# Kernel optimization log

Measured on AMD Instinct MI355X. Metric: run time of the kernel, lower is better.

Reference implementation:

```python
import jax, jax.numpy as jnp
import numpy as np

HIDDEN = 2048
N_HEADS = 16
N_KV_HEADS = 4
HEAD_DIM = HIDDEN // N_HEADS  # 128
BATCH = 2
SEQ = 2048


def setup_inputs() -> dict:
    key = jax.random.key(0)
    ks = jax.random.split(key, 10)
    s = 0.02
    return {
        "hidden_states": jax.random.normal(ks[0], (BATCH, SEQ, HIDDEN), jnp.float32),
        "attention_mask": jnp.ones((BATCH, SEQ), jnp.int32),
        # weights stored [in, out] so y = x @ W + b (transpose of torch layout)
        "Wq": jax.random.normal(ks[1], (HIDDEN, N_HEADS * HEAD_DIM), jnp.float32) * s,
        "bq": jnp.zeros((N_HEADS * HEAD_DIM,), jnp.float32),
        "Wk": jax.random.normal(ks[2], (HIDDEN, N_KV_HEADS * HEAD_DIM), jnp.float32) * s,
        "bk": jnp.zeros((N_KV_HEADS * HEAD_DIM,), jnp.float32),
        "Wv": jax.random.normal(ks[3], (HIDDEN, N_KV_HEADS * HEAD_DIM), jnp.float32) * s,
        "bv": jnp.zeros((N_KV_HEADS * HEAD_DIM,), jnp.float32),
        "Wo": jax.random.normal(ks[4], (N_HEADS * HEAD_DIM, HIDDEN), jnp.float32) * s,
        "bo": jnp.zeros((HIDDEN,), jnp.float32),
    }


def reference(hidden_states, attention_mask, Wq, bq, Wk, bk, Wv, bv, Wo, bo):
    B, S, _ = hidden_states.shape
    q = hidden_states @ Wq + bq  # [B,S,H*D]
    k = hidden_states @ Wk + bk  # [B,S,Hkv*D]
    v = hidden_states @ Wv + bv

    q = q.reshape(B, S, N_HEADS, HEAD_DIM).transpose(0, 2, 1, 3)      # [B,H,S,D]
    k = k.reshape(B, S, N_KV_HEADS, HEAD_DIM).transpose(0, 2, 1, 3)   # [B,Hkv,S,D]
    v = v.reshape(B, S, N_KV_HEADS, HEAD_DIM).transpose(0, 2, 1, 3)

    # GQA: repeat_interleave along head dim (head h uses kv head h // groups)
    groups = N_HEADS // N_KV_HEADS
    k = jnp.repeat(k, groups, axis=1)  # [B,H,S,D]
    v = jnp.repeat(v, groups, axis=1)

    scale = 1.0 / np.sqrt(HEAD_DIM)
    scores = jnp.einsum('bhqd,bhkd->bhqk', q, k) * scale  # [B,H,S,S]

    causal = jnp.tril(jnp.ones((S, S), bool))              # True = keep
    keep = causal[None, None, :, :] & (attention_mask[:, None, None, :] != 0)
    scores = jnp.where(keep, scores, -jnp.inf)

    attn = jax.nn.softmax(scores.astype(jnp.float32), axis=-1).astype(q.dtype)
    out = jnp.einsum('bhqk,bhkd->bhqd', attn, v)            # [B,H,S,D]
    out = out.transpose(0, 2, 1, 3).reshape(B, S, N_HEADS * HEAD_DIM)
    return out @ Wo + bo
```

## Files before the change

kernel.cpp:

```cpp
#include <hip/hip_runtime.h>
#include <hip/hip_bf16.h>


typedef unsigned short u16;
typedef unsigned long long u64;
typedef __attribute__((ext_vector_type(8))) short short8;
typedef __attribute__((ext_vector_type(4))) float f32x4;
typedef __attribute__((ext_vector_type(4))) unsigned uint4v;

#define BATCH 2
#define SEQ 2048
#define HIDDEN 2048
#define NH 16
#define NKV 4
#define HD 128
#define QKV_N 3072
#define MROWS 4096

__device__ inline u16 f2bf(float f) {
    __hip_bfloat16 h = __float2bfloat16(f);
    return __builtin_bit_cast(u16, h);
}

__device__ inline void async_copy16(const u16* g, u16* lds_base) {
    __builtin_amdgcn_global_load_lds(
        (const __attribute__((address_space(1))) void*)g,
        (__attribute__((address_space(3))) void*)lds_base, 16, 0, 0);
}

#define PREP_CONV   4096
#define PREP_WQ     (PREP_CONV + 1024)
#define PREP_WK     (PREP_WQ + 256)
#define PREP_WV     (PREP_WK + 256)
#define PREP_WO     (PREP_WV + 1024)
#define PREP_BIAS   (PREP_WO + 12)
#define PREP_TOTAL  (PREP_BIAS + 1)

__device__ inline void prep_transpose64(const float* __restrict__ src, u16* __restrict__ dst,
                                        int N, int sub, float (*tl)[69]) {
    int nx = N >> 6;
    int bx = sub % nx, by = sub / nx;
    int n0 = bx * 64, k0 = by * 64;
    int t = threadIdx.x;
    int rr = t >> 4, cc = (t & 15) * 4;
#pragma unroll
    for (int j = 0; j < 4; ++j) {
        float4 v = *(const float4*)(src + (size_t)(k0 + rr + 16 * j) * N + n0 + cc);
        int k = rr + 16 * j;
        tl[cc + 0][k] = v.x;
        tl[cc + 1][k] = v.y;
        tl[cc + 2][k] = v.z;
        tl[cc + 3][k] = v.w;
    }
    __syncthreads();
    int n = t >> 2;
#pragma unroll
    for (int j = 0; j < 2; ++j) {
        int kk = (t & 3) * 8 + 32 * j;
        short8 o8;
#pragma unroll
        for (int i = 0; i < 8; ++i) o8[i] = (short)f2bf(tl[n][kk + i]);
        *(short8*)(dst + (size_t)(n0 + n) * HIDDEN + k0 + kk) = o8;
    }
}

__global__ __launch_bounds__(256)
void prep(const float* __restrict__ hidden, u16* __restrict__ xb,
          const float* __restrict__ Wq, const float* __restrict__ Wk,
          const float* __restrict__ Wv, const float* __restrict__ Wo,
          u16* __restrict__ wqkvT, u16* __restrict__ woT,
          const float* __restrict__ bq, const float* __restrict__ bk,
          const float* __restrict__ bv, float* __restrict__ bqkv,
          const int* __restrict__ am, u64* __restrict__ mp) {
    __shared__ float tl[64][69];
    int bid = blockIdx.x;
    if (bid < PREP_CONV) {
        int i = (bid * 256 + threadIdx.x) * 8;
        float4 v0 = *(const float4*)(hidden + i);
        float4 v1 = *(const float4*)(hidden + i + 4);
        short8 o8;
        o8[0] = (short)f2bf(v0.x); o8[1] = (short)f2bf(v0.y);
        o8[2] = (short)f2bf(v0.z); o8[3] = (short)f2bf(v0.w);
        o8[4] = (short)f2bf(v1.x); o8[5] = (short)f2bf(v1.y);
        o8[6] = (short)f2bf(v1.z); o8[7] = (short)f2bf(v1.w);
        *(short8*)(xb + i) = o8;
    } else if (bid < PREP_WQ) {
        prep_transpose64(Wq, wqkvT, 2048, bid - PREP_CONV, tl);
    } else if (bid < PREP_WK) {
        prep_transpose64(Wk, wqkvT + (size_t)2048 * HIDDEN, 512, bid - PREP_WQ, tl);
    } else if (bid < PREP_WV) {
        prep_transpose64(Wv, wqkvT + (size_t)2560 * HIDDEN, 512, bid - PREP_WK, tl);
    } else if (bid < PREP_WO) {
        prep_transpose64(Wo, woT, 2048, bid - PREP_WV, tl);
    } else if (bid < PREP_BIAS) {
        int i = (bid - PREP_WO) * 256 + threadIdx.x;
        if (i < QKV_N)
            bqkv[i] = (i < 2048) ? bq[i] : ((i < 2560) ? bk[i - 2048] : bv[i - 2560]);
    } else {
        int i = threadIdx.x;
        if (i < BATCH * SEQ / 64) {
            const int* a = am + i * 64;
            u64 m = 0;
#pragma unroll
            for (int j = 0; j < 64; j += 4) {
                int4 v = *(const int4*)(a + j);
                m |= ((u64)(v.x != 0) << j) | ((u64)(v.y != 0) << (j + 1)) |
                     ((u64)(v.z != 0) << (j + 2)) | ((u64)(v.w != 0) << (j + 3));
            }
            mp[i] = m;
        }
    }
}

__global__ void vt_from_qkv(const u16* __restrict__ qkv, u16* __restrict__ vt) {
    __shared__ u16 tile[32][33];
    int b = blockIdx.z >> 2, kvh = blockIdx.z & 3;
    int s0 = blockIdx.x * 32, d0 = blockIdx.y * 32;
    int tx = threadIdx.x, ty = threadIdx.y;
#pragma unroll
    for (int i = 0; i < 32; i += 8)
        tile[ty + i][tx] = qkv[(size_t)(b * SEQ + s0 + ty + i) * QKV_N + 2560 + kvh * HD + d0 + tx];
    __syncthreads();
#pragma unroll
    for (int i = 0; i < 32; i += 8)
        vt[(size_t)((b * NKV + kvh) * HD + d0 + ty + i) * SEQ + s0 + tx] = tile[tx][ty + i];
}

template <bool OUT_BF16>
__global__ __launch_bounds__(512, 2)
void gemm_bf16_256(const u16* __restrict__ A, const u16* __restrict__ BT,
                   const float* __restrict__ bias, void* __restrict__ outp,
                   int M, int N, int K) {
    __shared__ __align__(16) u16 smem[2][2][256][64];
    const int t = threadIdx.x, w = t >> 6, lane = t & 63;
    const int quad = lane >> 4, l16 = lane & 15;
    const int wm = w >> 2, wn = w & 3;
    const int bm0 = blockIdx.y * 256, bn0 = blockIdx.x * 256;
    const int lrow = lane >> 3;
    const int lchk = (lane & 7) ^ lrow;
    const int NT = K >> 6;

    f32x4 acc[8][4];
#pragma unroll
    for (int i = 0; i < 8; i++)
#pragma unroll
        for (int j = 0; j < 4; j++) acc[i][j] = (f32x4){0.f, 0.f, 0.f, 0.f};

    const u16* gA = A + (size_t)bm0 * K;
    const u16* gB = BT + (size_t)bn0 * K;

    auto stage = [&](int buf, int op, int h, int k0) {
        const u16* gb = op ? gB : gA;
#pragma unroll
        for (int l = 0; l < 2; ++l) {
            int rb = h * 128 + w * 16 + l * 8;
            async_copy16(gb + (size_t)(rb + lrow) * K + k0 + lchk * 8,
                         &smem[buf][op][rb][0]);
        }
    };
    auto readA = [&](short8 (&aq)[4][2], int buf, int mh) {
#pragma unroll
        for (int mt = 0; mt < 4; ++mt) {
            int row = mh * 128 + mt * 32 + wm * 16 + l16;
            int swz = row & 7;
#pragma unroll
            for (int kk = 0; kk < 2; ++kk) {
                int chunk = ((kk << 2) | quad) ^ swz;
                aq[mt][kk] = *(const short8*)(&smem[buf][0][row][chunk << 3]);
            }
        }
    };
    auto readB = [&](short8 (&bq)[2][2], int buf, int nh) {
#pragma unroll
        for (int nt = 0; nt < 2; ++nt) {
            int row = nh * 128 + nt * 64 + wn * 16 + l16;
            int swz = row & 7;
#pragma unroll
            for (int kk = 0; kk < 2; ++kk) {
                int chunk = ((kk << 2) | quad) ^ swz;
                bq[nt][kk] = *(const short8*)(&smem[buf][1][row][chunk << 3]);
            }
        }
    };
    auto mmaQ = [&](short8 (&aq)[4][2], short8 (&bq)[2][2], int mh, int nh) {
        __builtin_amdgcn_s_setprio(1);
#pragma unroll
        for (int mt = 0; mt < 4; ++mt)
#pragma unroll
            for (int nt = 0; nt < 2; ++nt)
#pragma unroll
                for (int kk = 0; kk < 2; ++kk)
                    acc[mh * 4 + mt][nh * 2 + nt] = __builtin_amdgcn_mfma_f32_16x16x32_bf16(
                        aq[mt][kk], bq[nt][kk], acc[mh * 4 + mt][nh * 2 + nt], 0, 0, 0);
        __builtin_amdgcn_s_setprio(0);
    };

    stage(0, 0, 0, 0); stage(0, 1, 0, 0); stage(0, 1, 1, 0); stage(0, 0, 1, 0);
    asm volatile("s_waitcnt vmcnt(4)" ::: "memory");
    __builtin_amdgcn_s_barrier();

    short8 aq[4][2], b0[2][2], b1[2][2];
    for (int tt = 0; tt < NT - 1; ++tt) {
        const int cur = tt & 1, nxt = cur ^ 1, k1 = (tt + 1) << 6;
        readA(aq, cur, 0); readB(b0, cur, 0);
        stage(nxt, 0, 0, k1);
        mmaQ(aq, b0, 0, 0);
        asm volatile("s_waitcnt vmcnt(4)" ::: "memory");
        __builtin_amdgcn_s_barrier();
        readB(b1, cur, 1);
        stage(nxt, 1, 0, k1);
        mmaQ(aq, b1, 0, 1);
        asm volatile("s_waitcnt vmcnt(4)" ::: "memory");
        __builtin_amdgcn_s_barrier();
        readA(aq, cur, 1);
        stage(nxt, 1, 1, k1);
        mmaQ(aq, b1, 1, 1);
        asm volatile("s_waitcnt vmcnt(6)" ::: "memory");
        __builtin_amdgcn_s_barrier();
        stage(nxt, 0, 1, k1);
        mmaQ(aq, b0, 1, 0);
        asm volatile("s_waitcnt vmcnt(4)" ::: "memory");
        __builtin_amdgcn_s_barrier();
    }
    asm volatile("s_waitcnt vmcnt(0)" ::: "memory");
    __builtin_amdgcn_s_barrier();
    {
        const int cur = (NT - 1) & 1;
        readA(aq, cur, 0); readB(b0, cur, 0);
        mmaQ(aq, b0, 0, 0);
        readB(b1, cur, 1);
        mmaQ(aq, b1, 0, 1);
        readA(aq, cur, 1);
        mmaQ(aq, b1, 1, 1);
        mmaQ(aq, b0, 1, 0);
    }

#pragma unroll
    for (int nt = 0; nt < 4; ++nt) {
        int col = bn0 + nt * 64 + wn * 16 + l16;
        float bcol = bias[col];
#pragma unroll
        for (int mt = 0; mt < 8; ++mt) {
#pragma unroll
            for (int r = 0; r < 4; ++r) {
                int row = bm0 + mt * 32 + wm * 16 + quad * 4 + r;
                float v = acc[mt][nt][r] + bcol;
                if constexpr (OUT_BF16)
                    ((u16*)outp)[(size_t)row * N + col] = f2bf(v);
                else
                    ((float*)outp)[(size_t)row * N + col] = v;
            }
        }
    }
}

__global__ __launch_bounds__(512, 4)
void flash_attn(const u16* __restrict__ qkv, const u16* __restrict__ vt,
                const u64* __restrict__ mp, u16* __restrict__ attn) {
    __shared__ __align__(16) u16 Ks[64][136];
    __shared__ __align__(16) u16 Vs[128][72];
    int t = threadIdx.x, w = t >> 6, lane = t & 63, quad = lane >> 4, l16 = lane & 15;
    int bx = blockIdx.x, b = blockIdx.z;
    int qt = b ? ((int)gridDim.x - 1 - bx) : bx;
    int h = blockIdx.y, kvh = h >> 2;
    int q_row0 = qt * 128 + w * 16;

    const u16* qrow = qkv + (size_t)(b * SEQ + q_row0 + l16) * QKV_N + h * HD;
    short8 qf[4];
#pragma unroll
    for (int c = 0; c < 4; c++) qf[c] = *(const short8*)(qrow + c * 32 + quad * 8);

    f32x4 o[8];
#pragma unroll
    for (int dt = 0; dt < 8; dt++) o[dt] = (f32x4){0.f, 0.f, 0.f, 0.f};
    float lpart = 0.f;

    const float scale2 = 0.12751743f;
    const float C2 = 14.4269504f;

    const u16* kgb = qkv + (size_t)(b * SEQ) * QKV_N + 2048 + kvh * HD;
    const u16* vgb = vt + (size_t)((b * NKV + kvh) * HD) * SEQ;
    const u64* mpb = mp + b * (SEQ / 64);

    int kr = t >> 4, kc = (t & 15) * 8;
    int vr = t >> 3, vc = (t & 7) * 8;
    int kb_end = (qt + 1) * 128;

    short8 k0p, k1p, v0p, v1p;
    {
        k0p = *(const short8*)(kgb + (size_t)kr * QKV_N + kc);
        k1p = *(const short8*)(kgb + (size_t)(kr + 32) * QKV_N + kc);
        v0p = *(const short8*)(vgb + (size_t)vr * SEQ + vc);
        v1p = *(const short8*)(vgb + (size_t)(vr + 64) * SEQ + vc);
    }

    for (int kb = 0; kb < kb_end; kb += 64) {
        __syncthreads();
        *(short8*)(&Ks[kr][kc]) = k0p;
        *(short8*)(&Ks[kr + 32][kc]) = k1p;
        *(short8*)(&Vs[vr][vc]) = v0p;
        *(short8*)(&Vs[vr + 64][vc]) = v1p;
        __syncthreads();
        if (kb + 64 < kb_end) {
            const u16* kg = kgb + (size_t)(kb + 64) * QKV_N;
            const u16* vg = vgb + kb + 64;
            k0p = *(const short8*)(kg + (size_t)kr * QKV_N + kc);
            k1p = *(const short8*)(kg + (size_t)(kr + 32) * QKV_N + kc);
            v0p = *(const short8*)(vg + (size_t)vr * SEQ + vc);
            v1p = *(const short8*)(vg + (size_t)(vr + 64) * SEQ + vc);
        }
        if (kb > q_row0 + 15) continue;

        u64 mk = mpb[kb >> 6];

        f32x4 sc[4];
#pragma unroll
        for (int nt = 0; nt < 4; nt++) sc[nt] = (f32x4){0.f, 0.f, 0.f, 0.f};
        __builtin_amdgcn_s_setprio(1);
#pragma unroll
        for (int c = 0; c < 4; c++) {
#pragma unroll
            for (int nt = 0; nt < 4; nt++) {
                short8 kf = *(const short8*)(&Ks[nt * 16 + l16][c * 32 + quad * 8]);
                sc[nt] = __builtin_amdgcn_mfma_f32_16x16x32_bf16(kf, qf[c], sc[nt], 0, 0, 0);
            }
        }
        __builtin_amdgcn_s_setprio(0);

        short8 vf0a[4];
#pragma unroll
        for (int dt = 0; dt < 4; dt++)
            vf0a[dt] = *(const short8*)(&Vs[dt * 16 + l16][quad * 8]);

        float p[4][4];
        if (mk == ~0ull && kb + 63 <= q_row0) {
#pragma unroll
            for (int nt = 0; nt < 4; nt++)
#pragma unroll
                for (int r = 0; r < 4; r++)
                    p[nt][r] = __builtin_exp2f(__builtin_fmaf(sc[nt][r], scale2, -C2));
        } else {
            int limit = q_row0 + l16 - kb;
#pragma unroll
            for (int nt = 0; nt < 4; nt++) {
                unsigned nib = (unsigned)(mk >> (nt * 16 + quad * 4));
#pragma unroll
                for (int r = 0; r < 4; r++) {
                    int bp = nt * 16 + quad * 4 + r;
                    bool ok = ((nib >> r) & 1u) && (bp <= limit);
                    float v = ok ? sc[nt][r] : -INFINITY;
                    p[nt][r] = __builtin_exp2f(__builtin_fmaf(v, scale2, -C2));
                }
            }
        }
        lpart += ((p[0][0] + p[0][1]) + (p[0][2] + p[0][3])) +
                 ((p[1][0] + p[1][1]) + (p[1][2] + p[1][3])) +
                 ((p[2][0] + p[2][1]) + (p[2][2] + p[2][3])) +
                 ((p[3][0] + p[3][1]) + (p[3][2] + p[3][3]));

        unsigned A0, A1, B0, B1, C0, C1, E0, E1;
        asm("v_cvt_pk_bf16_f32 %0, %1, %2" : "=v"(A0) : "v"(p[0][0]), "v"(p[0][1]));
        asm("v_cvt_pk_bf16_f32 %0, %1, %2" : "=v"(A1) : "v"(p[0][2]), "v"(p[0][3]));
        asm("v_cvt_pk_bf16_f32 %0, %1, %2" : "=v"(B0) : "v"(p[1][0]), "v"(p[1][1]));
        asm("v_cvt_pk_bf16_f32 %0, %1, %2" : "=v"(B1) : "v"(p[1][2]), "v"(p[1][3]));
        asm("v_cvt_pk_bf16_f32 %0, %1, %2" : "=v"(C0) : "v"(p[2][0]), "v"(p[2][1]));
        asm("v_cvt_pk_bf16_f32 %0, %1, %2" : "=v"(C1) : "v"(p[2][2]), "v"(p[2][3]));
        asm("v_cvt_pk_bf16_f32 %0, %1, %2" : "=v"(E0) : "v"(p[3][0]), "v"(p[3][1]));
        asm("v_cvt_pk_bf16_f32 %0, %1, %2" : "=v"(E1) : "v"(p[3][2]), "v"(p[3][3]));
        asm("v_permlane32_swap_b32 %0, %1" : "+v"(A0), "+v"(B0));
        asm("v_permlane16_swap_b32 %0, %1" : "+v"(A0), "+v"(B0));
        asm("v_permlane32_swap_b32 %0, %1" : "+v"(A1), "+v"(B1));
        asm("v_permlane16_swap_b32 %0, %1" : "+v"(A1), "+v"(B1));
        asm("v_permlane32_swap_b32 %0, %1" : "+v"(C0), "+v"(E0));
        asm("v_permlane16_swap_b32 %0, %1" : "+v"(C0), "+v"(E0));
        asm("v_permlane32_swap_b32 %0, %1" : "+v"(C1), "+v"(E1));
        asm("v_permlane16_swap_b32 %0, %1" : "+v"(C1), "+v"(E1));
        short8 pf0 = __builtin_bit_cast(short8, (uint4v){A0, A1, B0, B1});
        short8 pf1 = __builtin_bit_cast(short8, (uint4v){C0, C1, E0, E1});

        __builtin_amdgcn_s_setprio(1);
#pragma unroll
        for (int dt = 0; dt < 4; dt++)
            o[dt] = __builtin_amdgcn_mfma_f32_16x16x32_bf16(pf0, vf0a[dt], o[dt], 0, 0, 0);
#pragma unroll
        for (int dt = 4; dt < 8; dt++) {
            short8 vf0 = *(const short8*)(&Vs[dt * 16 + l16][quad * 8]);
            o[dt] = __builtin_amdgcn_mfma_f32_16x16x32_bf16(pf0, vf0, o[dt], 0, 0, 0);
        }
#pragma unroll
        for (int dt = 0; dt < 8; dt++) {
            short8 vf1 = *(const short8*)(&Vs[dt * 16 + l16][32 + quad * 8]);
            o[dt] = __builtin_amdgcn_mfma_f32_16x16x32_bf16(pf1, vf1, o[dt], 0, 0, 0);
        }
        __builtin_amdgcn_s_setprio(0);
    }
    float l = lpart;
    l += __shfl_xor(l, 16, 64);
    l += __shfl_xor(l, 32, 64);
    float invq[4];
#pragma unroll
    for (int r = 0; r < 4; r++) {
        float lr = __shfl(l, quad * 4 + r, 16);
        invq[r] = lr > 0.f ? 1.f / lr : 0.f;
    }
    size_t obase = (size_t)(b * SEQ + q_row0) * HIDDEN + h * HD;
#pragma unroll
    for (int dt = 0; dt < 8; dt++)
#pragma unroll
        for (int r = 0; r < 4; r++)
            attn[obase + (size_t)(quad * 4 + r) * HIDDEN + dt * 16 + l16] =
                f2bf(o[dt][r] * invq[r]);
}

extern "C" void kernel_launch(void* const* d_in, const int* in_sizes, int n_in,
                              void* d_out, int out_size, void* d_ws, size_t ws_size,
                              hipStream_t stream) {
    const float* hidden = (const float*)d_in[0];
    const int* amask   = (const int*)d_in[1];
    const float* Wq = (const float*)d_in[2];
    const float* bq = (const float*)d_in[3];
    const float* Wk = (const float*)d_in[4];
    const float* bk = (const float*)d_in[5];
    const float* Wv = (const float*)d_in[6];
    const float* bv = (const float*)d_in[7];
    const float* Wo = (const float*)d_in[8];
    const float* bo = (const float*)d_in[9];
    float* out = (float*)d_out;

    char* ws = (char*)d_ws;
    u16* xb     = (u16*)ws;  ws += (size_t)MROWS * HIDDEN * 2;
    u16* wqkvT  = (u16*)ws;  ws += (size_t)QKV_N * HIDDEN * 2;
    u16* woT    = (u16*)ws;  ws += (size_t)HIDDEN * HIDDEN * 2;
    float* bqkv = (float*)ws; ws += (size_t)QKV_N * 4;
    u64* mpk    = (u64*)ws;  ws += (size_t)(MROWS / 64) * 8;
    u16* qkv    = (u16*)ws;  ws += (size_t)MROWS * QKV_N * 2;
    u16* vt     = (u16*)ws;  ws += (size_t)BATCH * NKV * HD * SEQ * 2;
    u16* attn   = (u16*)ws;  ws += (size_t)MROWS * HIDDEN * 2;

    prep<<<dim3(PREP_TOTAL), dim3(256), 0, stream>>>(
        hidden, xb, Wq, Wk, Wv, Wo, wqkvT, woT, bq, bk, bv, bqkv, amask, mpk);

    gemm_bf16_256<true><<<dim3(QKV_N / 256, MROWS / 256), dim3(512), 0, stream>>>(
        xb, wqkvT, bqkv, qkv, MROWS, QKV_N, HIDDEN);

    vt_from_qkv<<<dim3(SEQ / 32, HD / 32, BATCH * NKV), dim3(32, 8), 0, stream>>>(qkv, vt);

    flash_attn<<<dim3(SEQ / 128, NH, BATCH), dim3(512), 0, stream>>>(qkv, vt, mpk, attn);

    gemm_bf16_256<false><<<dim3(HIDDEN / 256, MROWS / 256), dim3(512), 0, stream>>>(
        attn, woT, bo, out, MROWS, HIDDEN, HIDDEN);
}
```

Before: 293.3 us.

## Add 128x256 output GEMM and XOR-swizzle flash-attention LDS tiles

Adds a new 128x256-tile GEMM for the output projection. It uses double-buffered async LDS staging split into two N-halves with swizzled chunks. The smaller M tile doubles the grid from 128 to 256 blocks, which should fill more CUs on the final projection. Separately, the flash-attention K and V shared tiles drop their padding in favour of an XOR swizzle, which cuts LDS use and aims to avoid bank conflicts on the fragment reads. The new GEMM reloads each B tile across more M blocks, and the swizzle indexing adds a few ALU ops.

```diff
diff --git a/kernel.cpp b/kernel.cpp
--- a/kernel.cpp
+++ b/kernel.cpp
@@ -254,16 +254,134 @@
     }
 }
 
+__global__ __launch_bounds__(512, 2)
+void gemm_bf16_128x256(const u16* __restrict__ A, const u16* __restrict__ BT,
+                       const float* __restrict__ bias, float* __restrict__ outp,
+                       int M, int N, int K) {
+    __shared__ __align__(16) u16 sA[2][128][64];
+    __shared__ __align__(16) u16 sB[2][256][64];
+    const int t = threadIdx.x, w = t >> 6, lane = t & 63;
+    const int quad = lane >> 4, l16 = lane & 15;
+    const int wm = w >> 2, wn = w & 3;
+    const int bm0 = blockIdx.y * 128, bn0 = blockIdx.x * 256;
+    const int lrow = lane >> 3;
+    const int lchk = (lane & 7) ^ lrow;
+    const int NT = K >> 6;
+
+    f32x4 acc[4][4];
+#pragma unroll
+    for (int i = 0; i < 4; i++)
+#pragma unroll
+        for (int j = 0; j < 4; j++) acc[i][j] = (f32x4){0.f, 0.f, 0.f, 0.f};
+
+    const u16* gA = A + (size_t)bm0 * K;
+    const u16* gB = BT + (size_t)bn0 * K;
+
+    auto stageA = [&](int buf, int k0) {
+#pragma unroll
+        for (int l = 0; l < 2; ++l) {
+            int rb = w * 16 + l * 8;
+            async_copy16(gA + (size_t)(rb + lrow) * K + k0 + lchk * 8, &sA[buf][rb][0]);
+        }
+    };
+    auto stageB = [&](int buf, int h, int k0) {
+#pragma unroll
+        for (int l = 0; l < 2; ++l) {
+            int rb = h * 128 + w * 16 + l * 8;
+            async_copy16(gB + (size_t)(rb + lrow) * K + k0 + lchk * 8, &sB[buf][rb][0]);
+        }
+    };
+    auto readA = [&](short8 (&aq)[4][2], int buf) {
+#pragma unroll
+        for (int mt = 0; mt < 4; ++mt) {
+            int row = wm * 64 + mt * 16 + l16;
+            int swz = row & 7;
+#pragma unroll
+            for (int kk = 0; kk < 2; ++kk) {
+                int chunk = ((kk << 2) | quad) ^ swz;
+                aq[mt][kk] = *(const short8*)(&sA[buf][row][chunk << 3]);
+            }
+        }
+    };
+    auto readB = [&](short8 (&bq)[2][2], int buf, int nh) {
+#pragma unroll
+        for (int nt = 0; nt < 2; ++nt) {
+            int row = nh * 128 + nt * 64 + wn * 16 + l16;
+            int swz = row & 7;
+#pragma unroll
+            for (int kk = 0; kk < 2; ++kk) {
+                int chunk = ((kk << 2) | quad) ^ swz;
+                bq[nt][kk] = *(const short8*)(&sB[buf][row][chunk << 3]);
+            }
+        }
+    };
+    auto mmaH = [&](short8 (&aq)[4][2], short8 (&bq)[2][2], int nh) {
+        __builtin_amdgcn_s_setprio(1);
+#pragma unroll
+        for (int mt = 0; mt < 4; ++mt)
+#pragma unroll
+            for (int nt = 0; nt < 2; ++nt)
+#pragma unroll
+                for (int kk = 0; kk < 2; ++kk)
+                    acc[mt][nh * 2 + nt] = __builtin_amdgcn_mfma_f32_16x16x32_bf16(
+                        aq[mt][kk], bq[nt][kk], acc[mt][nh * 2 + nt], 0, 0, 0);
+        __builtin_amdgcn_s_setprio(0);
+    };
+
+    stageA(0, 0); stageB(0, 0, 0); stageB(0, 1, 0);
+    asm volatile("s_waitcnt vmcnt(2)" ::: "memory");
+    __builtin_amdgcn_s_barrier();
+
+    short8 aq[4][2], b0[2][2], b1[2][2];
+    for (int tt = 0; tt < NT - 1; ++tt) {
+        const int cur = tt & 1, nxt = cur ^ 1, k1 = (tt + 1) << 6;
+        readA(aq, cur); readB(b0, cur, 0);
+        stageA(nxt, k1); stageB(nxt, 0, k1);
+        mmaH(aq, b0, 0);
+        asm volatile("s_waitcnt vmcnt(4)" ::: "memory");
+        __builtin_amdgcn_s_barrier();
+        readB(b1, cur, 1);
+        stageB(nxt, 1, k1);
+        mmaH(aq, b1, 1);
+        asm volatile("s_waitcnt vmcnt(2)" ::: "memory");
+        __builtin_amdgcn_s_barrier();
+    }
+    asm volatile("s_waitcnt vmcnt(0)" ::: "memory");
+    __builtin_amdgcn_s_barrier();
+    {
+        const int cur = (NT - 1) & 1;
+        readA(aq, cur); readB(b0, cur, 0);
+        mmaH(aq, b0, 0);
+        readB(b1, cur, 1);
+        mmaH(aq, b1, 1);
+    }
+
+#pragma unroll
+    for (int j = 0; j < 4; ++j) {
+        int col = bn0 + j * 64 + wn * 16 + l16;
+        float bcol = bias[col];
+#pragma unroll
+        for (int mt = 0; mt < 4; ++mt) {
+#pragma unroll
+            for (int r = 0; r < 4; ++r) {
+                int row = bm0 + wm * 64 + mt * 16 + quad * 4 + r;
+                outp[(size_t)row * N + col] = acc[mt][j][r] + bcol;
+            }
+        }
+    }
+}
+
 __global__ __launch_bounds__(512, 4)
 void flash_attn(const u16* __restrict__ qkv, const u16* __restrict__ vt,
                 const u64* __restrict__ mp, u16* __restrict__ attn) {
-    __shared__ __align__(16) u16 Ks[64][136];
-    __shared__ __align__(16) u16 Vs[128][72];
+    __shared__ __align__(16) u16 Ks[64][128];
+    __shared__ __align__(16) u16 Vs[128][64];
     int t = threadIdx.x, w = t >> 6, lane = t & 63, quad = lane >> 4, l16 = lane & 15;
     int bx = blockIdx.x, b = blockIdx.z;
     int qt = b ? ((int)gridDim.x - 1 - bx) : bx;
     int h = blockIdx.y, kvh = h >> 2;
     int q_row0 = qt * 128 + w * 16;
+    int s7 = l16 & 7;
 
     const u16* qrow = qkv + (size_t)(b * SEQ + q_row0 + l16) * QKV_N + h * HD;
     short8 qf[4];
@@ -283,7 +401,9 @@
     const u64* mpb = mp + b * (SEQ / 64);
 
     int kr = t >> 4, kc = (t & 15) * 8;
+    int kpos = ((t & 15) ^ (kr & 7)) * 8;
     int vr = t >> 3, vc = (t & 7) * 8;
+    int vpos = ((t & 7) ^ (vr & 7)) * 8;
     int kb_end = (qt + 1) * 128;
 
     short8 k0p, k1p, v0p, v1p;
@@ -296,10 +416,10 @@
 
     for (int kb = 0; kb < kb_end; kb += 64) {
         __syncthreads();
-        *(short8*)(&Ks[kr][kc]) = k0p;
-        *(short8*)(&Ks[kr + 32][kc]) = k1p;
-        *(short8*)(&Vs[vr][vc]) = v0p;
-        *(short8*)(&Vs[vr + 64][vc]) = v1p;
+        *(short8*)(&Ks[kr][kpos]) = k0p;
+        *(short8*)(&Ks[kr + 32][kpos]) = k1p;
+        *(short8*)(&Vs[vr][vpos]) = v0p;
+        *(short8*)(&Vs[vr + 64][vpos]) = v1p;
         __syncthreads();
         if (kb + 64 < kb_end) {
             const u16* kg = kgb + (size_t)(kb + 64) * QKV_N;
@@ -321,7 +441,7 @@
         for (int c = 0; c < 4; c++) {
 #pragma unroll
             for (int nt = 0; nt < 4; nt++) {
-                short8 kf = *(const short8*)(&Ks[nt * 16 + l16][c * 32 + quad * 8]);
+                short8 kf = *(const short8*)(&Ks[nt * 16 + l16][(((c << 2) | quad) ^ s7) << 3]);
                 sc[nt] = __builtin_amdgcn_mfma_f32_16x16x32_bf16(kf, qf[c], sc[nt], 0, 0, 0);
             }
         }
@@ -330,7 +450,7 @@
         short8 vf0a[4];
 #pragma unroll
         for (int dt = 0; dt < 4; dt++)
-            vf0a[dt] = *(const short8*)(&Vs[dt * 16 + l16][quad * 8]);
+            vf0a[dt] = *(const short8*)(&Vs[dt * 16 + l16][(quad ^ s7) << 3]);
 
         float p[4][4];
         if (mk == ~0ull && kb + 63 <= q_row0) {
@@ -384,12 +504,12 @@
             o[dt] = __builtin_amdgcn_mfma_f32_16x16x32_bf16(pf0, vf0a[dt], o[dt], 0, 0, 0);
 #pragma unroll
         for (int dt = 4; dt < 8; dt++) {
-            short8 vf0 = *(const short8*)(&Vs[dt * 16 + l16][quad * 8]);
+            short8 vf0 = *(const short8*)(&Vs[dt * 16 + l16][(quad ^ s7) << 3]);
             o[dt] = __builtin_amdgcn_mfma_f32_16x16x32_bf16(pf0, vf0, o[dt], 0, 0, 0);
         }
 #pragma unroll
         for (int dt = 0; dt < 8; dt++) {
-            short8 vf1 = *(const short8*)(&Vs[dt * 16 + l16][32 + quad * 8]);
+            short8 vf1 = *(const short8*)(&Vs[dt * 16 + l16][((4 | quad) ^ s7) << 3]);
             o[dt] = __builtin_amdgcn_mfma_f32_16x16x32_bf16(pf1, vf1, o[dt], 0, 0, 0);
         }
         __builtin_amdgcn_s_setprio(0);
@@ -447,6 +567,6 @@
 
     flash_attn<<<dim3(SEQ / 128, NH, BATCH), dim3(512), 0, stream>>>(qkv, vt, mpk, attn);
 
-    gemm_bf16_256<false><<<dim3(HIDDEN / 256, MROWS / 256), dim3(512), 0, stream>>>(
+    gemm_bf16_128x256<<<dim3(HIDDEN / 256, MROWS / 128), dim3(512), 0, stream>>>(
         attn, woT, bo, out, MROWS, HIDDEN, HIDDEN);
 }
```

Result: slower. 310.1 us (+5.7%).
